# Performance work log

Hardware: AMD Instinct MI355X
Metric: run time of the kernel (lower is better)

## Reference

```python
import jax, jax.numpy as jnp
import numpy as np

INPUT_SIZE = 2048
HIDDEN_SIZE = 4096
NUM_CLASSES = 1000
BATCH = 4096


def setup_inputs() -> dict:
    key = jax.random.key(0)
    kx, k1, k2, k3 = jax.random.split(key, 4)
    x = jax.random.normal(kx, (BATCH, INPUT_SIZE), dtype=jnp.float32)
    w1 = jax.random.normal(k1, (INPUT_SIZE, HIDDEN_SIZE), dtype=jnp.float32) * 0.01
    b1 = jnp.zeros((HIDDEN_SIZE,), dtype=jnp.float32)
    w2 = jax.random.normal(k2, (HIDDEN_SIZE, HIDDEN_SIZE), dtype=jnp.float32) * 0.01
    b2 = jnp.zeros((HIDDEN_SIZE,), dtype=jnp.float32)
    w3 = jax.random.normal(k3, (HIDDEN_SIZE, NUM_CLASSES), dtype=jnp.float32) * 0.01
    b3 = jnp.zeros((NUM_CLASSES,), dtype=jnp.float32)
    return {"x": x, "w1": w1, "b1": b1, "w2": w2, "b2": b2, "w3": w3, "b3": b3}


def reference(x, w1, b1, w2, b2, w3, b3):
    # fused GEMM + bias + ReLU, equivalent to the original Python double-loop matmul
    h1 = jax.nn.relu(x @ w1 + b1)    # [B, H]
    h2 = jax.nn.relu(h1 @ w2 + b2)   # [B, H]
    out = h2 @ w3 + b3               # [B, C]
    return out
```

## Files before the change

### kernel.cpp

```cpp
#include <hip/hip_runtime.h>
#include <hip/hip_bf16.h>

typedef __bf16 bf16x8 __attribute__((ext_vector_type(8)));
typedef __bf16 bf16x4 __attribute__((ext_vector_type(4)));
typedef float floatx4 __attribute__((ext_vector_type(4)));

#define B_    4096
#define IN_   2048
#define HID_  4096
#define NC_   1000
#define NCP_  1024

__device__ __forceinline__ void transpose_cvt_dev(const float* __restrict__ src,
                                                  __bf16* __restrict__ dst,
                                                  int R, int C, int bx, int by,
                                                  float* tile ) {
    const int r0 = bx * 64;
    const int c0 = by * 64;
    const int t  = threadIdx.x;
#pragma unroll
    for (int it = 0; it < 4; ++it) {
        int lin = it * 256 + t;
        int sr = lin >> 4, c4 = lin & 15;
        int cb = c0 + c4 * 4;
        const float* s = src + (size_t)(r0 + sr) * C;
        float4 v;
        if (cb + 3 < C) {
            v = *(const float4*)(s + cb);
        } else {
            v.x = (cb + 0 < C) ? s[cb + 0] : 0.f;
            v.y = (cb + 1 < C) ? s[cb + 1] : 0.f;
            v.z = (cb + 2 < C) ? s[cb + 2] : 0.f;
            v.w = (cb + 3 < C) ? s[cb + 3] : 0.f;
        }
        tile[(c4 * 4 + 0) * 65 + sr] = v.x;
        tile[(c4 * 4 + 1) * 65 + sr] = v.y;
        tile[(c4 * 4 + 2) * 65 + sr] = v.z;
        tile[(c4 * 4 + 3) * 65 + sr] = v.w;
    }
    __syncthreads();
#pragma unroll
    for (int it = 0; it < 2; ++it) {
        int lin = it * 256 + t;
        int dr = lin >> 3, q8 = lin & 7;
        bf16x8 o;
#pragma unroll
        for (int j = 0; j < 8; ++j) o[j] = (__bf16)tile[dr * 65 + q8 * 8 + j];
        *(bf16x8*)(dst + (size_t)(c0 + dr) * R + r0 + q8 * 8) = o;
    }
}

template <bool RELU, bool OUT_BF16>
__device__ __forceinline__ void gemm_core(const __bf16* __restrict__ A,
                                          const __bf16* __restrict__ Bt,
                                          const float* __restrict__ bias,
                                          void* __restrict__ Cv,
                                          int M, int K, int Nstore,
                                          int bx, int by,
                                          __bf16* sA, __bf16* sB) {
    const int tid   = threadIdx.x;
    const int lane  = tid & 63;
    const int wave  = tid >> 6;
    const int wr    = wave >> 1;
    const int wc    = wave & 1;
    const int mBase = by * 128;
    const int nBase = bx * 128;
    const int lr    = lane >> 4;
    const int lc    = lane & 15;

    floatx4 acc[4][4];
#pragma unroll
    for (int i = 0; i < 4; ++i)
#pragma unroll
        for (int j = 0; j < 4; ++j) acc[i][j] = (floatx4)0.f;

    for (int k0 = 0; k0 < K; k0 += 64) {
#pragma unroll
        for (int it = 0; it < 4; ++it) {
            int lin = it * 256 + tid;
            int r   = lin >> 3;
            int kc  = (lin & 7) ^ (r & 7);
            const __bf16* ga = A  + (size_t)(mBase + r) * K + k0 + kc * 8;
            const __bf16* gb = Bt + (size_t)(nBase + r) * K + k0 + kc * 8;
            __builtin_amdgcn_global_load_lds(
                (__attribute__((address_space(1))) void*)ga,
                (__attribute__((address_space(3))) void*)(sA + lin * 8), 16, 0, 0);
            __builtin_amdgcn_global_load_lds(
                (__attribute__((address_space(1))) void*)gb,
                (__attribute__((address_space(3))) void*)(sB + lin * 8), 16, 0, 0);
        }
        __builtin_amdgcn_s_waitcnt(0);
        __syncthreads();

#pragma unroll
        for (int kk = 0; kk < 2; ++kk) {
            const int sw = (kk * 4 + lr) ^ (lc & 7);
            bf16x8 af[4], bfr[4];
#pragma unroll
            for (int i = 0; i < 4; ++i)
                af[i] = *(const bf16x8*)(sA + (wr * 64 + i * 16 + lc) * 64 + sw * 8);
#pragma unroll
            for (int j = 0; j < 4; ++j)
                bfr[j] = *(const bf16x8*)(sB + (wc * 64 + j * 16 + lc) * 64 + sw * 8);
#pragma unroll
            for (int i = 0; i < 4; ++i)
#pragma unroll
                for (int j = 0; j < 4; ++j)
                    acc[i][j] = __builtin_amdgcn_mfma_f32_16x16x32_bf16(af[i], bfr[j], acc[i][j], 0, 0, 0);
        }
        __syncthreads();
    }

#pragma unroll
    for (int j = 0; j < 4; ++j) {
        int col = nBase + wc * 64 + j * 16 + lc;
        if (col < Nstore) {
            float bv = bias[col];
#pragma unroll
            for (int i = 0; i < 4; ++i) {
                int rowb = mBase + wr * 64 + i * 16 + lr * 4;
#pragma unroll
                for (int r = 0; r < 4; ++r) {
                    float v = acc[i][j][r] + bv;
                    if (RELU) v = fmaxf(v, 0.f);
                    if (OUT_BF16)
                        ((__bf16*)Cv)[(size_t)(rowb + r) * Nstore + col] = (__bf16)v;
                    else
                        ((float*)Cv)[(size_t)(rowb + r) * Nstore + col] = v;
                }
            }
        }
    }
}

__global__ __launch_bounds__(256) void prep1(const float* __restrict__ x,
                                             __bf16* __restrict__ xb,
                                             const float* __restrict__ w1,
                                             __bf16* __restrict__ w1t) {
    __shared__ float tile[64 * 65];
    const int b = blockIdx.x;
    if (b < 4096) {
        int i = (b * 256 + (int)threadIdx.x) * 8;
        float4 a = *(const float4*)(x + i);
        float4 c = *(const float4*)(x + i + 4);
        bf16x8 o;
        o[0] = (__bf16)a.x; o[1] = (__bf16)a.y; o[2] = (__bf16)a.z; o[3] = (__bf16)a.w;
        o[4] = (__bf16)c.x; o[5] = (__bf16)c.y; o[6] = (__bf16)c.z; o[7] = (__bf16)c.w;
        *(bf16x8*)(xb + i) = o;
    } else {
        int l = b - 4096;
        transpose_cvt_dev(w1, w1t, IN_, HID_, l & 31, l >> 5, tile);
    }
}

__global__ __launch_bounds__(256, 2) void gemm1_fused(const __bf16* __restrict__ xb,
                                                      const __bf16* __restrict__ w1t,
                                                      const float* __restrict__ b1,
                                                      __bf16* __restrict__ h1,
                                                      const float* __restrict__ w2,
                                                      __bf16* __restrict__ w2t,
                                                      const float* __restrict__ w3,
                                                      __bf16* __restrict__ w3t) {
    __shared__ float smem[8192];
    const int b = blockIdx.x;
    if (b < 1024) {
        __bf16* sA = (__bf16*)smem;
        __bf16* sB = sA + 128 * 64;
        gemm_core<true, true>(xb, w1t, b1, h1, B_, IN_, HID_, b & 31, b >> 5, sA, sB);
    } else if (b < 5120) {
        int l = b - 1024;
        transpose_cvt_dev(w2, w2t, HID_, HID_, l & 63, l >> 6, smem);
    } else {
        int l = b - 5120;
        transpose_cvt_dev(w3, w3t, HID_, NC_, l & 63, l >> 6, smem);
    }
}

template <bool RELU, bool OUT_BF16>
__global__ __launch_bounds__(256, 2) void gemm_bt(const __bf16* __restrict__ A,
                                                  const __bf16* __restrict__ Bt,
                                                  const float* __restrict__ bias,
                                                  void* __restrict__ Cv,
                                                  int M, int K, int Nstore) {
    __shared__ __bf16 sA[128 * 64];
    __shared__ __bf16 sB[128 * 64];
    gemm_core<RELU, OUT_BF16>(A, Bt, bias, Cv, M, K, Nstore,
                              blockIdx.x, blockIdx.y, sA, sB);
}

extern "C" void kernel_launch(void* const* d_in, const int* in_sizes, int n_in,
                              void* d_out, int out_size, void* d_ws, size_t ws_size,
                              hipStream_t stream) {
    const float* x  = (const float*)d_in[0];
    const float* w1 = (const float*)d_in[1];
    const float* b1 = (const float*)d_in[2];
    const float* w2 = (const float*)d_in[3];
    const float* b2 = (const float*)d_in[4];
    const float* w3 = (const float*)d_in[5];
    const float* b3 = (const float*)d_in[6];
    float* out = (float*)d_out;

    char* ws = (char*)d_ws;
    __bf16* xb  = (__bf16*)(ws);
    __bf16* w1t = (__bf16*)(ws + (16u << 20));
    __bf16* w2t = (__bf16*)(ws + (32u << 20));
    __bf16* w3t = (__bf16*)(ws + (64u << 20));
    __bf16* h1  = (__bf16*)(ws + (72u << 20));
    __bf16* h2  = (__bf16*)(ws);

    prep1<<<6144, 256, 0, stream>>>(x, xb, w1, w1t);

    gemm1_fused<<<6144, 256, 0, stream>>>(xb, w1t, b1, h1, w2, w2t, w3, w3t);

    gemm_bt<true, true><<<dim3(HID_ / 128, B_ / 128), 256, 0, stream>>>(
        h1, w2t, b2, h2, B_, HID_, HID_);

    gemm_bt<false, false><<<dim3(NCP_ / 128, B_ / 128), 256, 0, stream>>>(
        h2, w3t, b3, out, B_, HID_, NC_);
}
```

Baseline: 423.5 us.

## Double-buffer GEMM K-loop with BK=32 and split-K the final layer

Rewrites the shared GEMM core to use a 32-wide K tile with two LDS buffers, so the next tile's global-to-LDS load is issued before the MFMAs on the current tile, with one barrier per iteration. It also splits the last GEMM (output 4096x1024) into two K halves to double its block count, writing fp32 partials to workspace that a separate kernel sums with the bias. The aim is to hide load latency and fill more CUs on the small final GEMM. The cost is an extra kernel launch and partial-sum traffic. The prefetch has no explicit wait before the next iteration's reads beyond the barrier, which may rely on implicit waitcnt behaviour.

Result: slower. 467.2 us (+10.3%).

```diff
diff --git a/kernel.cpp b/kernel.cpp
--- a/kernel.cpp
+++ b/kernel.cpp
@@ -10,6 +10,10 @@
 #define HID_  4096
 #define NC_   1000
 #define NCP_  1024
+
+#define GLDS(g, l) __builtin_amdgcn_global_load_lds(                         \
+    (__attribute__((address_space(1))) void*)(g),                            \
+    (__attribute__((address_space(3))) void*)(l), 16, 0, 0)
 
 __device__ __forceinline__ void transpose_cvt_dev(const float* __restrict__ src,
                                                   __bf16* __restrict__ dst,
@@ -56,7 +60,7 @@
                                           const float* __restrict__ bias,
                                           void* __restrict__ Cv,
                                           int M, int K, int Nstore,
-                                          int bx, int by,
+                                          int bx, int by, int kBeg, int kEnd,
                                           __bf16* sA, __bf16* sB) {
     const int tid   = threadIdx.x;
     const int lane  = tid & 63;
@@ -68,54 +72,68 @@
     const int lr    = lane >> 4;
     const int lc    = lane & 15;
 
+    const int lin0 = tid, lin1 = 256 + tid;
+    const int r0s = lin0 >> 2, c0s = (lin0 & 3) ^ ((r0s >> 1) & 3);
+    const int r1s = lin1 >> 2, c1s = (lin1 & 3) ^ ((r1s >> 1) & 3);
+    const __bf16* gA0 = A  + (size_t)(mBase + r0s) * K + kBeg + c0s * 8;
+    const __bf16* gA1 = A  + (size_t)(mBase + r1s) * K + kBeg + c1s * 8;
+    const __bf16* gB0 = Bt + (size_t)(nBase + r0s) * K + kBeg + c0s * 8;
+    const __bf16* gB1 = Bt + (size_t)(nBase + r1s) * K + kBeg + c1s * 8;
+
+    int offA[4], offB[4];
+#pragma unroll
+    for (int i = 0; i < 4; ++i) {
+        int rowA = wr * 64 + i * 16 + lc;
+        offA[i] = rowA * 32 + (lr ^ ((rowA >> 1) & 3)) * 8;
+        int rowB = wc * 64 + i * 16 + lc;
+        offB[i] = rowB * 32 + (lr ^ ((rowB >> 1) & 3)) * 8;
+    }
+
     floatx4 acc[4][4];
 #pragma unroll
     for (int i = 0; i < 4; ++i)
 #pragma unroll
         for (int j = 0; j < 4; ++j) acc[i][j] = (floatx4)0.f;
 
-    for (int k0 = 0; k0 < K; k0 += 64) {
-#pragma unroll
-        for (int it = 0; it < 4; ++it) {
-            int lin = it * 256 + tid;
-            int r   = lin >> 3;
-            int kc  = (lin & 7) ^ (r & 7);
-            const __bf16* ga = A  + (size_t)(mBase + r) * K + k0 + kc * 8;
-            const __bf16* gb = Bt + (size_t)(nBase + r) * K + k0 + kc * 8;
-            __builtin_amdgcn_global_load_lds(
-                (__attribute__((address_space(1))) void*)ga,
-                (__attribute__((address_space(3))) void*)(sA + lin * 8), 16, 0, 0);
-            __builtin_amdgcn_global_load_lds(
-                (__attribute__((address_space(1))) void*)gb,
-                (__attribute__((address_space(3))) void*)(sB + lin * 8), 16, 0, 0);
+    GLDS(gA0, sA + lin0 * 8);
+    GLDS(gA1, sA + lin1 * 8);
+    GLDS(gB0, sB + lin0 * 8);
+    GLDS(gB1, sB + lin1 * 8);
+    gA0 += 32; gA1 += 32; gB0 += 32; gB1 += 32;
+    __builtin_amdgcn_s_waitcnt(0);
+    __syncthreads();
+
+    const int nIter = (kEnd - kBeg) >> 5;
+    int p = 0;
+    for (int itk = 0; itk < nIter; ++itk) {
+        if (itk + 1 < nIter) {
+            const int q = (p ^ 1) * 4096;
+            GLDS(gA0, sA + q + lin0 * 8);
+            GLDS(gA1, sA + q + lin1 * 8);
+            GLDS(gB0, sB + q + lin0 * 8);
+            GLDS(gB1, sB + q + lin1 * 8);
+            gA0 += 32; gA1 += 32; gB0 += 32; gB1 += 32;
         }
-        __builtin_amdgcn_s_waitcnt(0);
+        const int pb = p * 4096;
+        bf16x8 af[4], bfr[4];
+#pragma unroll
+        for (int i = 0; i < 4; ++i) af[i]  = *(const bf16x8*)(sA + pb + offA[i]);
+#pragma unroll
+        for (int j = 0; j < 4; ++j) bfr[j] = *(const bf16x8*)(sB + pb + offB[j]);
+#pragma unroll
+        for (int i = 0; i < 4; ++i)
+#pragma unroll
+            for (int j = 0; j < 4; ++j)
+                acc[i][j] = __builtin_amdgcn_mfma_f32_16x16x32_bf16(af[i], bfr[j], acc[i][j], 0, 0, 0);
         __syncthreads();
-
-#pragma unroll
-        for (int kk = 0; kk < 2; ++kk) {
-            const int sw = (kk * 4 + lr) ^ (lc & 7);
-            bf16x8 af[4], bfr[4];
-#pragma unroll
-            for (int i = 0; i < 4; ++i)
-                af[i] = *(const bf16x8*)(sA + (wr * 64 + i * 16 + lc) * 64 + sw * 8);
-#pragma unroll
-            for (int j = 0; j < 4; ++j)
-                bfr[j] = *(const bf16x8*)(sB + (wc * 64 + j * 16 + lc) * 64 + sw * 8);
-#pragma unroll
-            for (int i = 0; i < 4; ++i)
-#pragma unroll
-                for (int j = 0; j < 4; ++j)
-                    acc[i][j] = __builtin_amdgcn_mfma_f32_16x16x32_bf16(af[i], bfr[j], acc[i][j], 0, 0, 0);
-        }
-        __syncthreads();
+        p ^= 1;
     }
 
 #pragma unroll
     for (int j = 0; j < 4; ++j) {
         int col = nBase + wc * 64 + j * 16 + lc;
         if (col < Nstore) {
-            float bv = bias[col];
+            float bv = bias ? bias[col] : 0.f;
 #pragma unroll
             for (int i = 0; i < 4; ++i) {
                 int rowb = mBase + wr * 64 + i * 16 + lr * 4;
@@ -165,8 +183,9 @@
     const int b = blockIdx.x;
     if (b < 1024) {
         __bf16* sA = (__bf16*)smem;
-        __bf16* sB = sA + 128 * 64;
-        gemm_core<true, true>(xb, w1t, b1, h1, B_, IN_, HID_, b & 31, b >> 5, sA, sB);
+        __bf16* sB = sA + 8192;
+        gemm_core<true, true>(xb, w1t, b1, h1, B_, IN_, HID_,
+                              b & 31, b >> 5, 0, IN_, sA, sB);
     } else if (b < 5120) {
         int l = b - 1024;
         transpose_cvt_dev(w2, w2t, HID_, HID_, l & 63, l >> 6, smem);
@@ -182,10 +201,32 @@
                                                   const float* __restrict__ bias,
                                                   void* __restrict__ Cv,
                                                   int M, int K, int Nstore) {
-    __shared__ __bf16 sA[128 * 64];
-    __shared__ __bf16 sB[128 * 64];
+    __shared__ __bf16 sA[2 * 128 * 32];
+    __shared__ __bf16 sB[2 * 128 * 32];
     gemm_core<RELU, OUT_BF16>(A, Bt, bias, Cv, M, K, Nstore,
-                              blockIdx.x, blockIdx.y, sA, sB);
+                              blockIdx.x, blockIdx.y, 0, K, sA, sB);
+}
+
+__global__ __launch_bounds__(256, 2) void gemm_sk(const __bf16* __restrict__ A,
+                                                  const __bf16* __restrict__ Bt,
+                                                  float* __restrict__ P,
+                                                  int M, int KH, int Ktot) {
+    __shared__ __bf16 sA[2 * 128 * 32];
+    __shared__ __bf16 sB[2 * 128 * 32];
+    const int z = blockIdx.z;
+    float* Pz = P + (size_t)z * M * NCP_;
+    gemm_core<false, false>(A, Bt, (const float*)nullptr, Pz, M, Ktot, NCP_,
+                            blockIdx.x, blockIdx.y, z * KH, (z + 1) * KH, sA, sB);
+}
+
+__global__ __launch_bounds__(256) void reduce_bias(const float* __restrict__ P,
+                                                   const float* __restrict__ b3,
+                                                   float* __restrict__ out) {
+    int c = blockIdx.x * 256 + threadIdx.x;
+    int m = blockIdx.y;
+    if (c < NC_)
+        out[(size_t)m * NC_ + c] =
+            P[(size_t)m * NCP_ + c] + P[(size_t)(B_ + m) * NCP_ + c] + b3[c];
 }
 
 extern "C" void kernel_launch(void* const* d_in, const int* in_sizes, int n_in,
@@ -207,6 +248,7 @@
     __bf16* w3t = (__bf16*)(ws + (64u << 20));
     __bf16* h1  = (__bf16*)(ws + (72u << 20));
     __bf16* h2  = (__bf16*)(ws);
+    float*  P   = (float*)(ws + (72u << 20));
 
     prep1<<<6144, 256, 0, stream>>>(x, xb, w1, w1t);
 
@@ -215,6 +257,7 @@
     gemm_bt<true, true><<<dim3(HID_ / 128, B_ / 128), 256, 0, stream>>>(
         h1, w2t, b2, h2, B_, HID_, HID_);
 
-    gemm_bt<false, false><<<dim3(NCP_ / 128, B_ / 128), 256, 0, stream>>>(
-        h2, w3t, b3, out, B_, HID_, NC_);
-}
+    gemm_sk<<<dim3(NCP_ / 128, B_ / 128, 2), 256, 0, stream>>>(
+        h2, w3t, P, B_, HID_ / 2, HID_);
+    reduce_bias<<<dim3(NCP_ / 256, B_), 256, 0, stream>>>(P, b3, out);
+}
```
